# Performance work log

Hardware: AMD Instinct MI355X
Metric: run time of the kernel (lower is better)

The kernel has to match this reference:

```python
import jax, jax.numpy as jnp
import numpy as np

V, E, G, D = 30000, 60000, 1200, 64
NODE_IN, EDGE_IN, EH = 74, 12, 128
N_MP, N_S2S, N_LSTM = 6, 6, 3


def setup_inputs() -> dict:
    key = jax.random.key(0)
    ks = iter(jax.random.split(key, 48))
    def rn(shape, s=0.05):
        return jax.random.normal(next(ks), shape, dtype=jnp.float32) * s
    inp = {
        "node_feats": jax.random.normal(next(ks), (V, NODE_IN), dtype=jnp.float32),
        "edge_feats": jax.random.normal(next(ks), (E, EDGE_IN), dtype=jnp.float32),
        "src": jax.random.randint(next(ks), (E,), 0, V, dtype=jnp.int32),
        "dst": jax.random.randint(next(ks), (E,), 0, V, dtype=jnp.int32),
        "node_graph_ids": jnp.sort(jax.random.randint(next(ks), (V,), 0, G, dtype=jnp.int32)),
        # MPNNGNN: node projection, edge network, NNConv bias, GRU
        "proj_W": rn((NODE_IN, D)), "proj_b": rn((D,)),
        "eW1": rn((EDGE_IN, EH)), "eb1": rn((EH,)),
        "eW2": rn((EH, D * D)), "eb2": rn((D * D,)),
        "conv_b": rn((D,)),
        "gru_Wih": rn((D, 3 * D)), "gru_bih": rn((3 * D,)),
        "gru_Whh": rn((D, 3 * D)), "gru_bhh": rn((3 * D,)),
        # process + predict MLPs
        "pW": rn((2 * D, D)), "pb": rn((D,)),
        "qW1": rn((D, D)), "qb1": rn((D,)),
        "qW2": rn((D, D)), "qb2": rn((D,)),
        "qW3": rn((D, 1)), "qb3": rn((1,)),
    }
    # Set2Set 3-layer LSTM: layer0 input 2D, layers 1-2 input D; gates i,f,g,o
    for l, din in enumerate([2 * D, D, D]):
        inp[f"lstm_Wih{l}"] = rn((din, 4 * D)); inp[f"lstm_bih{l}"] = rn((4 * D,))
        inp[f"lstm_Whh{l}"] = rn((D, 4 * D)); inp[f"lstm_bhh{l}"] = rn((4 * D,))
    return inp


def _forward(floats, src, dst, gids):
    (node_feats, edge_feats, proj_W, proj_b, eW1, eb1, eW2, eb2, conv_b,
     gru_Wih, gru_bih, gru_Whh, gru_bhh,
     lWih0, lbih0, lWhh0, lbhh0,
     lWih1, lbih1, lWhh1, lbhh1,
     lWih2, lbih2, lWhh2, lbhh2,
     pW, pb, qW1, qb1, qW2, qb2, qW3, qb3) = floats

    # ---- MPNNGNN ----
    h = jax.nn.relu(node_feats @ proj_W + proj_b)            # (V, D)
    hidden = h
    # per-edge weight matrices (edge_feats fixed across MP steps -> compute once)
    We = (jax.nn.relu(edge_feats @ eW1 + eb1) @ eW2 + eb2).reshape(E, D, D)
    for _ in range(N_MP):
        m = jnp.einsum('ei,eio->eo', h[src], We)             # (E, D)
        agg = jax.ops.segment_sum(m, dst, num_segments=V) + conv_b
        x = jax.nn.relu(agg)
        # PyTorch GRU cell
        gi = x @ gru_Wih + gru_bih
        gh = hidden @ gru_Whh + gru_bhh
        ir, iz, inn = jnp.split(gi, 3, axis=-1)
        hr, hz, hn = jnp.split(gh, 3, axis=-1)
        r = jax.nn.sigmoid(ir + hr)
        z = jax.nn.sigmoid(iz + hz)
        n = jnp.tanh(inn + r * hn)
        h = (1.0 - z) * n + z * hidden
        hidden = h

    # ---- Set2Set readout ----
    lstm = [(lWih0, lbih0, lWhh0, lbhh0),
            (lWih1, lbih1, lWhh1, lbhh1),
            (lWih2, lbih2, lWhh2, lbhh2)]
    hs = [jnp.zeros((G, D), h.dtype) for _ in range(N_LSTM)]
    cs = [jnp.zeros((G, D), h.dtype) for _ in range(N_LSTM)]
    q_star = jnp.zeros((G, 2 * D), h.dtype)
    for _ in range(N_S2S):
        x = q_star
        nhs, ncs = [], []
        for l, (Wih, bih, Whh, bhh) in enumerate(lstm):
            gates = x @ Wih + bih + hs[l] @ Whh + bhh
            i_g, f_g, g_g, o_g = jnp.split(gates, 4, axis=-1)
            c = jax.nn.sigmoid(f_g) * cs[l] + jax.nn.sigmoid(i_g) * jnp.tanh(g_g)
            hh = jax.nn.sigmoid(o_g) * jnp.tanh(c)
            nhs.append(hh); ncs.append(c)
            x = hh
        hs, cs = nhs, ncs
        q = x                                               # (G, D)
        e = jnp.sum(h * q[gids], axis=-1)                   # (V,)
        emax = jax.ops.segment_max(e, gids, num_segments=G, indices_are_sorted=True)
        ex = jnp.exp(e - emax[gids])
        denom = jax.ops.segment_sum(ex, gids, num_segments=G, indices_are_sorted=True)
        alpha = ex / denom[gids]                            # per-graph softmax
        readout = jax.ops.segment_sum(h * alpha[:, None], gids, num_segments=G, indices_are_sorted=True)
        q_star = jnp.concatenate([q, readout], axis=-1)     # (G, 2D)

    # ---- process + predict MLPs (dropout = identity in eval) ----
    gf = jax.nn.relu(q_star @ pW + pb)
    y = jax.nn.relu(gf @ qW1 + qb1)
    y = jax.nn.relu(y @ qW2 + qb2)
    return y @ qW3 + qb3                                    # (G, 1)


def reference(node_feats, edge_feats, src, dst, node_graph_ids,
              proj_W, proj_b, eW1, eb1, eW2, eb2, conv_b,
              gru_Wih, gru_bih, gru_Whh, gru_bhh,
              lstm_Wih0, lstm_bih0, lstm_Whh0, lstm_bhh0,
              lstm_Wih1, lstm_bih1, lstm_Whh1, lstm_bhh1,
              lstm_Wih2, lstm_bih2, lstm_Whh2, lstm_bhh2,
              pW, pb, qW1, qb1, qW2, qb2, qW3, qb3):
    floats = (node_feats, edge_feats, proj_W, proj_b, eW1, eb1, eW2, eb2, conv_b,
              gru_Wih, gru_bih, gru_Whh, gru_bhh,
              lstm_Wih0, lstm_bih0, lstm_Whh0, lstm_bhh0,
              lstm_Wih1, lstm_bih1, lstm_Whh1, lstm_bhh1,
              lstm_Wih2, lstm_bih2, lstm_Whh2, lstm_bhh2,
              pW, pb, qW1, qb1, qW2, qb2, qW3, qb3)
    return _forward(floats, src, dst, node_graph_ids)
```

## Files before the change

### kernel.cpp

```cpp
#include <hip/hip_runtime.h>
#include <stdint.h>
#include <math.h>

#define V 30000
#define E 60000
#define G 1200
#define D 64
#define NODE_IN 74
#define EDGE_IN 12
#define EH 128
#define N_MP 6
#define N_S2S 6

#define NBLK ((E + 63) / 64)
#define EPAD (NBLK * 64)
#define GRUBLK ((V + 31) / 32)

typedef short bf16x8 __attribute__((ext_vector_type(8)));
typedef float f32x4 __attribute__((ext_vector_type(4)));

__device__ __forceinline__ float sigmoidf_(float x) {
    return 1.0f / (1.0f + __expf(-x));
}
__device__ __forceinline__ float tanhf_(float x) {
    float t = __expf(-2.0f * fabsf(x));
    float r = (1.0f - t) / (1.0f + t);
    return copysignf(r, x);
}
__device__ __forceinline__ uint16_t f2bf(float f) {
    uint32_t u = __float_as_uint(f);
    u += 0x7fffu + ((u >> 16) & 1u);
    return (uint16_t)(u >> 16);
}
__device__ __forceinline__ float bf2f(uint16_t u) {
    return __uint_as_float(((uint32_t)u) << 16);
}

__global__ void k_zero(float* __restrict__ p, int n4) {
    int i = blockIdx.x * blockDim.x + threadIdx.x;
    if (i < n4) ((float4*)p)[i] = make_float4(0.f, 0.f, 0.f, 0.f);
}

__global__ void k_node_proj(const float* __restrict__ nf, const float* __restrict__ W,
                            const float* __restrict__ b, float* __restrict__ h) {
    int wave = threadIdx.x >> 6, lane = threadIdx.x & 63;
    int v = blockIdx.x * 4 + wave;
    __shared__ float xs[4][NODE_IN];
    xs[wave][lane] = nf[(size_t)v * NODE_IN + lane];
    if (lane + 64 < NODE_IN) xs[wave][lane + 64] = nf[(size_t)v * NODE_IN + lane + 64];
    __syncthreads();
    float acc = b[lane];
    #pragma unroll
    for (int i = 0; i < NODE_IN; ++i) acc = fmaf(xs[wave][i], W[i * D + lane], acc);
    h[(size_t)v * D + lane] = fmaxf(acc, 0.0f);
}

__global__ __launch_bounds__(256) void k_edge_hidden(const float* __restrict__ ef,
                              const float* __restrict__ W1,
                              const float* __restrict__ b1, uint16_t* __restrict__ HedgeP) {
    int blk = blockIdx.x;
    int t = threadIdx.x;
    int half = t >> 7, j = t & 127;
    __shared__ float xs[8][EDGE_IN];
    if (t < 8 * EDGE_IN) {
        int el = t / EDGE_IN, c = t % EDGE_IN;
        int e = blk * 8 + el;
        xs[el][c] = (e < E) ? ef[(size_t)e * EDGE_IN + c] : 0.f;
    }
    __syncthreads();
    #pragma unroll
    for (int l = 0; l < 4; ++l) {
        int el = half * 4 + l;
        int e = blk * 8 + el;
        float acc = b1[j];
        #pragma unroll
        for (int i = 0; i < EDGE_IN; ++i) acc = fmaf(xs[el][i], W1[i * EH + j], acc);
        float r = (e < E) ? fmaxf(acc, 0.0f) : 0.0f;
        int bb = e >> 6, ww = (e >> 4) & 3, m = e & 15;
        int kt = j >> 5, quad = (j >> 3) & 3, jj = j & 7;
        size_t off = ((((size_t)(bb * 4 + ww) * 4 + kt) * 4 + quad) * 16 + m) * 8 + jj;
        HedgeP[off] = f2bf(r);
    }
}

__global__ void k_prep_w2(const float* __restrict__ eW2, uint16_t* __restrict__ W2p) {
    int idx = blockIdx.x * 256 + threadIdx.x;
    int j = idx & 7;
    int n0 = (idx >> 3) & 15;
    int quad = (idx >> 7) & 3;
    int nt = (idx >> 9) & 3;
    int kt = (idx >> 11) & 3;
    int i = idx >> 13;
    int k = kt * 32 + quad * 8 + j;
    int col = i * 64 + nt * 16 + n0;
    W2p[idx] = f2bf(eW2[(size_t)k * 4096 + col]);
}

__global__ void k_prep_b2(const float* __restrict__ eb2, uint16_t* __restrict__ B2p) {
    int idx = blockIdx.x * 256 + threadIdx.x;
    if (idx >= 4096) { B2p[idx] = 0; return; }
    int j = idx & 7;
    int n0 = (idx >> 3) & 15;
    int quad = (idx >> 7) & 3;
    int nt = (idx >> 9) & 3;
    int kb = (idx >> 11) & 1;
    B2p[idx] = f2bf(eb2[(size_t)(kb * 32 + quad * 8 + j) * 64 + nt * 16 + n0]);
}

__global__ void k_prep_wc(const float* __restrict__ Wih, const float* __restrict__ Whh,
                          const float* __restrict__ bih, const float* __restrict__ bhh,
                          uint16_t* __restrict__ Wcp, float* __restrict__ bc) {
    int idx = blockIdx.x * 256 + threadIdx.x;
    int j = idx & 7;
    int n0 = (idx >> 3) & 15;
    int quad = (idx >> 7) & 3;
    int kt = (idx >> 9) & 3;
    int ot = idx >> 11;
    int k = kt * 32 + quad * 8 + j;
    int c = ot * 16 + n0;
    float val = 0.f;
    if (c < 128) {
        val = (k < 64) ? Wih[(size_t)k * 192 + c] : Whh[(size_t)(k - 64) * 192 + c];
    } else if (c < 192) {
        if (k < 64) val = Wih[(size_t)k * 192 + c];
    } else {
        if (k >= 64) val = Whh[(size_t)(k - 64) * 192 + (c - 64)];
    }
    Wcp[idx] = f2bf(val);
    if (idx < 256) {
        int d = idx & 63;
        float b;
        if (idx < 64)       b = bih[d] + bhh[d];
        else if (idx < 128) b = bih[64 + d] + bhh[64 + d];
        else if (idx < 192) b = bih[128 + d];
        else                b = bhh[128 + d];
        bc[idx] = b;
    }
}

__global__ __launch_bounds__(256, 3) void k_message_mfma(
    const uint16_t* __restrict__ HedgeP, const uint16_t* __restrict__ W2p,
    const uint16_t* __restrict__ B2p, const float* __restrict__ h,
    const int* __restrict__ src, const int* __restrict__ dst,
    float* __restrict__ agg) {
    const int bx = blockIdx.x;
    const int b = bx >> 1;
    const int ibase = (bx & 1) * 32;
    const int t = threadIdx.x;
    const int w = t >> 6, lane = t & 63;
    const int quad = lane >> 4, n0 = lane & 15;

    __shared__ uint16_t HsU[64][72];
    __shared__ int srcv[64], dstv[64];

    if (t < 64) {
        int e = b * 64 + t;
        int sv = 0, dv = -1;
        if (e < E) { sv = src[e]; dv = dst[e]; }
        srcv[t] = sv; dstv[t] = dv;
    }
    __syncthreads();
    for (int idx = t; idx < 4096; idx += 256) {
        int r = idx >> 6, c = idx & 63;
        HsU[r][c] = f2bf(h[(size_t)srcv[r] * 64 + c]);
    }
    bf16x8 Af[4][4];
    #pragma unroll
    for (int et = 0; et < 4; ++et)
        #pragma unroll
        for (int kt = 0; kt < 4; ++kt)
            Af[et][kt] = *(const bf16x8*)(HedgeP + (((size_t)(b * 4 + et) * 4 + kt) * 512) + lane * 8);
    __syncthreads();

    f32x4 acc[4];
    {
        const uint16_t* b2b = B2p + (size_t)ibase * 128;
        bf16x8 B2f0 = *(const bf16x8*)(b2b + (size_t)(0 * 4 + w) * 512 + lane * 8);
        bf16x8 B2f1 = *(const bf16x8*)(b2b + (size_t)(1 * 4 + w) * 512 + lane * 8);
        #pragma unroll
        for (int et = 0; et < 4; ++et) {
            bf16x8 hA0 = *(const bf16x8*)(&HsU[et * 16 + n0][quad * 8]);
            bf16x8 hA1 = *(const bf16x8*)(&HsU[et * 16 + n0][32 + quad * 8]);
            f32x4 z = {};
            z = __builtin_amdgcn_mfma_f32_16x16x32_bf16(hA0, B2f0, z, 0, 0, 0);
            acc[et] = __builtin_amdgcn_mfma_f32_16x16x32_bf16(hA1, B2f1, z, 0, 0, 0);
        }
    }

    for (int ii = 0; ii < 32; ++ii) {
        const int i = ibase + ii;
        const uint16_t* wb = W2p + (size_t)i * 8192 + lane * 8;
        bf16x8 Bf0 = *(const bf16x8*)(wb + (size_t)(0 * 4 + w) * 512);
        bf16x8 Bf1 = *(const bf16x8*)(wb + (size_t)(1 * 4 + w) * 512);
        bf16x8 Bf2 = *(const bf16x8*)(wb + (size_t)(2 * 4 + w) * 512);
        bf16x8 Bf3 = *(const bf16x8*)(wb + (size_t)(3 * 4 + w) * 512);
        #pragma unroll
        for (int et = 0; et < 4; ++et) {
            f32x4 tmp = {};
            tmp = __builtin_amdgcn_mfma_f32_16x16x32_bf16(Af[et][0], Bf0, tmp, 0, 0, 0);
            tmp = __builtin_amdgcn_mfma_f32_16x16x32_bf16(Af[et][1], Bf1, tmp, 0, 0, 0);
            tmp = __builtin_amdgcn_mfma_f32_16x16x32_bf16(Af[et][2], Bf2, tmp, 0, 0, 0);
            tmp = __builtin_amdgcn_mfma_f32_16x16x32_bf16(Af[et][3], Bf3, tmp, 0, 0, 0);
            int r0 = et * 16 + quad * 4;
            acc[et][0] = fmaf(bf2f(HsU[r0 + 0][i]), tmp[0], acc[et][0]);
            acc[et][1] = fmaf(bf2f(HsU[r0 + 1][i]), tmp[1], acc[et][1]);
            acc[et][2] = fmaf(bf2f(HsU[r0 + 2][i]), tmp[2], acc[et][2]);
            acc[et][3] = fmaf(bf2f(HsU[r0 + 3][i]), tmp[3], acc[et][3]);
        }
    }

    #pragma unroll
    for (int et = 0; et < 4; ++et) {
        #pragma unroll
        for (int reg = 0; reg < 4; ++reg) {
            int d = dstv[et * 16 + quad * 4 + reg];
            if (d >= 0)
                atomicAdd(agg + (size_t)d * 64 + w * 16 + n0, acc[et][reg]);
        }
    }
}

__global__ __launch_bounds__(256) void k_gru_mfma(
    float* __restrict__ agg, const float* __restrict__ convb,
    const uint16_t* __restrict__ Wcp, const float* __restrict__ bc,
    float* __restrict__ hcur) {
    const int blk = blockIdx.x;
    const int v0 = blk * 32;
    const int t = threadIdx.x;
    const int w = t >> 6, lane = t & 63;
    const int quad = lane >> 4, n0 = lane & 15;

    __shared__ uint16_t As[32][136];
    __shared__ uint16_t Gs[32][264];

    for (int idx = t; idx < 2048; idx += 256) {
        int r = idx >> 6, c = idx & 63;
        int v = v0 + r;
        if (v < V) {
            size_t off = (size_t)v * 64 + c;
            float x = fmaxf(agg[off] + convb[c], 0.f);
            agg[off] = 0.f;
            As[r][c] = f2bf(x);
            As[r][64 + c] = f2bf(hcur[off]);
        } else {
            As[r][c] = 0; As[r][64 + c] = 0;
        }
    }
    __syncthreads();

    bf16x8 Af[2][4];
    #pragma unroll
    for (int et = 0; et < 2; ++et)
        #pragma unroll
        for (int kt = 0; kt < 4; ++kt)
            Af[et][kt] = *(const bf16x8*)(&As[et * 16 + n0][kt * 32 + quad * 8]);

    f32x4 acc[2][4] = {};
    #pragma unroll
    for (int ot4 = 0; ot4 < 4; ++ot4) {
        const uint16_t* wb = Wcp + (size_t)((w * 4 + ot4) * 4) * 512 + lane * 8;
        bf16x8 B0 = *(const bf16x8*)(wb + 0 * 512);
        bf16x8 B1 = *(const bf16x8*)(wb + 1 * 512);
        bf16x8 B2 = *(const bf16x8*)(wb + 2 * 512);
        bf16x8 B3 = *(const bf16x8*)(wb + 3 * 512);
        #pragma unroll
        for (int et = 0; et < 2; ++et) {
            f32x4 a = acc[et][ot4];
            a = __builtin_amdgcn_mfma_f32_16x16x32_bf16(Af[et][0], B0, a, 0, 0, 0);
            a = __builtin_amdgcn_mfma_f32_16x16x32_bf16(Af[et][1], B1, a, 0, 0, 0);
            a = __builtin_amdgcn_mfma_f32_16x16x32_bf16(Af[et][2], B2, a, 0, 0, 0);
            a = __builtin_amdgcn_mfma_f32_16x16x32_bf16(Af[et][3], B3, a, 0, 0, 0);
            acc[et][ot4] = a;
        }
    }
    #pragma unroll
    for (int et = 0; et < 2; ++et)
        #pragma unroll
        for (int ot4 = 0; ot4 < 4; ++ot4)
            #pragma unroll
            for (int reg = 0; reg < 4; ++reg)
                Gs[et * 16 + quad * 4 + reg][(w * 4 + ot4) * 16 + n0] = f2bf(acc[et][ot4][reg]);
    __syncthreads();

    for (int idx = t; idx < 2048; idx += 256) {
        int r = idx >> 6, d = idx & 63;
        int v = v0 + r;
        if (v >= V) continue;
        size_t off = (size_t)v * 64 + d;
        float rp   = bf2f(Gs[r][d])        + bc[d];
        float zp   = bf2f(Gs[r][64 + d])   + bc[64 + d];
        float innv = bf2f(Gs[r][128 + d])  + bc[128 + d];
        float hnv  = bf2f(Gs[r][192 + d])  + bc[192 + d];
        float hv = hcur[off];
        float rr = sigmoidf_(rp);
        float zz = sigmoidf_(zp);
        float nn = tanhf_(innv + rr * hnv);
        hcur[off] = (1.f - zz) * nn + zz * hv;
    }
}

__global__ void k_seg(const int* __restrict__ gids, int* __restrict__ start) {
    int v = blockIdx.x * blockDim.x + threadIdx.x;
    if (v > V) return;
    int cur = (v < V) ? gids[v] : G;
    int prev = (v == 0) ? -1 : gids[v - 1];
    for (int g = prev + 1; g <= cur; ++g) start[g] = v;
}

#define LS_GPB 8
__global__ __launch_bounds__(256) void k_lstm(const float* __restrict__ q_star,
    const float* __restrict__ Wih0, const float* __restrict__ bih0,
    const float* __restrict__ Whh0, const float* __restrict__ bhh0,
    const float* __restrict__ Wih1, const float* __restrict__ bih1,
    const float* __restrict__ Whh1, const float* __restrict__ bhh1,
    const float* __restrict__ Wih2, const float* __restrict__ bih2,
    const float* __restrict__ Whh2, const float* __restrict__ bhh2,
    float* __restrict__ hs, float* __restrict__ cs, float* __restrict__ q) {
    int g0 = blockIdx.x * LS_GPB;
    int j = threadIdx.x;
    __shared__ float xs[LS_GPB][128];
    __shared__ float hl[LS_GPB][64];
    __shared__ float gates[LS_GPB][256];
    for (int idx = j; idx < LS_GPB * 128; idx += 256) {
        int n = idx >> 7, d = idx & 127;
        xs[n][d] = q_star[(size_t)(g0 + n) * 128 + d];
    }
    const float* Wihs[3] = {Wih0, Wih1, Wih2};
    const float* bihs[3] = {bih0, bih1, bih2};
    const float* Whhs[3] = {Whh0, Whh1, Whh2};
    const float* bhhs[3] = {bhh0, bhh1, bhh2};
    const int dins[3] = {128, 64, 64};
    for (int l = 0; l < 3; ++l) {
        for (int idx = j; idx < LS_GPB * 64; idx += 256) {
            int n = idx >> 6, d = idx & 63;
            hl[n][d] = hs[(size_t)l * G * 64 + (size_t)(g0 + n) * 64 + d];
        }
        __syncthreads();
        float acc[LS_GPB];
        float bsum = bihs[l][j] + bhhs[l][j];
        #pragma unroll
        for (int n = 0; n < LS_GPB; ++n) acc[n] = bsum;
        const float* Wih = Wihs[l];
        int din = dins[l];
        for (int i = 0; i < din; ++i) {
            float w = Wih[i * 256 + j];
            #pragma unroll
            for (int n = 0; n < LS_GPB; ++n) acc[n] = fmaf(xs[n][i], w, acc[n]);
        }
        const float* Whh = Whhs[l];
        for (int i = 0; i < 64; ++i) {
            float w = Whh[i * 256 + j];
            #pragma unroll
            for (int n = 0; n < LS_GPB; ++n) acc[n] = fmaf(hl[n][i], w, acc[n]);
        }
        #pragma unroll
        for (int n = 0; n < LS_GPB; ++n) gates[n][j] = acc[n];
        __syncthreads();
        for (int idx = j; idx < LS_GPB * 64; idx += 256) {
            int n = idx >> 6, d = idx & 63;
            float ig = gates[n][d], fg = gates[n][64 + d];
            float gt = gates[n][128 + d], og = gates[n][192 + d];
            size_t off = (size_t)l * G * 64 + (size_t)(g0 + n) * 64 + d;
            float c = sigmoidf_(fg) * cs[off] + sigmoidf_(ig) * tanhf_(gt);
            float hnew = sigmoidf_(og) * tanhf_(c);
            cs[off] = c;
            hs[off] = hnew;
            xs[n][d] = hnew;
            if (l == 2) q[(size_t)(g0 + n) * 64 + d] = hnew;
        }
        __syncthreads();
    }
}

__global__ void k_attention(const float* __restrict__ h, const float* __restrict__ q,
                            const int* __restrict__ segs, float* __restrict__ q_star) {
    int g = blockIdx.x;
    int lane = threadIdx.x;
    int vs = segs[g], ve = segs[g + 1];
    float qv = q[(size_t)g * 64 + lane];
    float m = -INFINITY;
    for (int v = vs; v < ve; ++v) {
        float p = h[(size_t)v * 64 + lane] * qv;
        #pragma unroll
        for (int off = 32; off > 0; off >>= 1) p += __shfl_xor(p, off, 64);
        m = fmaxf(m, p);
    }
    float s = 0.f, acc = 0.f;
    for (int v = vs; v < ve; ++v) {
        float hv = h[(size_t)v * 64 + lane];
        float p = hv * qv;
        #pragma unroll
        for (int off = 32; off > 0; off >>= 1) p += __shfl_xor(p, off, 64);
        float ex = __expf(p - m);
        s += ex;
        acc = fmaf(hv, ex, acc);
    }
    float r = (ve > vs) ? acc / s : 0.f;
    q_star[(size_t)g * 128 + lane] = qv;
    q_star[(size_t)g * 128 + 64 + lane] = r;
}

__global__ void k_final(const float* __restrict__ q_star,
                        const float* __restrict__ pW, const float* __restrict__ pb,
                        const float* __restrict__ qW1, const float* __restrict__ qb1,
                        const float* __restrict__ qW2, const float* __restrict__ qb2,
                        const float* __restrict__ qW3, const float* __restrict__ qb3,
                        float* __restrict__ out) {
    int g = blockIdx.x;
    int lane = threadIdx.x;
    __shared__ float buf[128];
    buf[lane] = q_star[(size_t)g * 128 + lane];
    buf[64 + lane] = q_star[(size_t)g * 128 + 64 + lane];
    __syncthreads();
    float y = pb[lane];
    #pragma unroll 8
    for (int i = 0; i < 128; ++i) y = fmaf(buf[i], pW[i * 64 + lane], y);
    y = fmaxf(y, 0.f);
    __syncthreads(); buf[lane] = y; __syncthreads();
    float y1 = qb1[lane];
    #pragma unroll 8
    for (int i = 0; i < 64; ++i) y1 = fmaf(buf[i], qW1[i * 64 + lane], y1);
    y1 = fmaxf(y1, 0.f);
    __syncthreads(); buf[lane] = y1; __syncthreads();
    float y2 = qb2[lane];
    #pragma unroll 8
    for (int i = 0; i < 64; ++i) y2 = fmaf(buf[i], qW2[i * 64 + lane], y2);
    y2 = fmaxf(y2, 0.f);
    float p = y2 * qW3[lane];
    #pragma unroll
    for (int off = 32; off > 0; off >>= 1) p += __shfl_xor(p, off, 64);
    if (lane == 0) out[g] = p + qb3[0];
}

extern "C" void kernel_launch(void* const* d_in, const int* in_sizes, int n_in,
                              void* d_out, int out_size, void* d_ws, size_t ws_size,
                              hipStream_t stream) {
    const float* node_feats = (const float*)d_in[0];
    const float* edge_feats = (const float*)d_in[1];
    const int*   src        = (const int*)d_in[2];
    const int*   dst        = (const int*)d_in[3];
    const int*   gids       = (const int*)d_in[4];
    const float* proj_W     = (const float*)d_in[5];
    const float* proj_b     = (const float*)d_in[6];
    const float* eW1        = (const float*)d_in[7];
    const float* eb1        = (const float*)d_in[8];
    const float* eW2        = (const float*)d_in[9];
    const float* eb2        = (const float*)d_in[10];
    const float* conv_b     = (const float*)d_in[11];
    const float* gru_Wih    = (const float*)d_in[12];
    const float* gru_bih    = (const float*)d_in[13];
    const float* gru_Whh    = (const float*)d_in[14];
    const float* gru_bhh    = (const float*)d_in[15];
    const float* pW         = (const float*)d_in[16];
    const float* pb         = (const float*)d_in[17];
    const float* qW1        = (const float*)d_in[18];
    const float* qb1        = (const float*)d_in[19];
    const float* qW2        = (const float*)d_in[20];
    const float* qb2        = (const float*)d_in[21];
    const float* qW3        = (const float*)d_in[22];
    const float* qb3        = (const float*)d_in[23];
    const float* lWih0 = (const float*)d_in[24]; const float* lbih0 = (const float*)d_in[25];
    const float* lWhh0 = (const float*)d_in[26]; const float* lbhh0 = (const float*)d_in[27];
    const float* lWih1 = (const float*)d_in[28]; const float* lbih1 = (const float*)d_in[29];
    const float* lWhh1 = (const float*)d_in[30]; const float* lbhh1 = (const float*)d_in[31];
    const float* lWih2 = (const float*)d_in[32]; const float* lbih2 = (const float*)d_in[33];
    const float* lWhh2 = (const float*)d_in[34]; const float* lbhh2 = (const float*)d_in[35];

    char* ws = (char*)d_ws;
    uint16_t* HedgeP = (uint16_t*)(ws + 0);
    uint16_t* W2p    = (uint16_t*)(ws + 15368192);
    uint16_t* B2p    = (uint16_t*)(ws + 16416768);
    float*    hcur   = (float*)(ws + 16433152);
    float*    agg    = (float*)(ws + 24113152);
    float*    q_star = (float*)(ws + 31793152);
    float*    hsbuf  = (float*)(ws + 32407552);
    float*    csbuf  = (float*)(ws + 33329152);
    float*    qbuf   = (float*)(ws + 34250752);
    int*      segs   = (int*)(ws + 34557952);
    uint16_t* Wcp    = (uint16_t*)hsbuf;
    float*    bc     = (float*)(ws + 32407552 + 65536);

    k_node_proj<<<V / 4, 256, 0, stream>>>(node_feats, proj_W, proj_b, hcur);
    k_edge_hidden<<<EPAD / 8, 256, 0, stream>>>(edge_feats, eW1, eb1, HedgeP);
    k_prep_w2<<<2048, 256, 0, stream>>>(eW2, W2p);
    k_prep_b2<<<32, 256, 0, stream>>>(eb2, B2p);
    k_prep_wc<<<128, 256, 0, stream>>>(gru_Wih, gru_Whh, gru_bih, gru_bhh, Wcp, bc);
    k_seg<<<(V + 1 + 255) / 256, 256, 0, stream>>>(gids, segs);
    k_zero<<<(480000 + 255) / 256, 256, 0, stream>>>(agg, 480000);

    for (int t = 0; t < N_MP; ++t) {
        k_message_mfma<<<NBLK * 2, 256, 0, stream>>>(HedgeP, W2p, B2p, hcur, src, dst, agg);
        k_gru_mfma<<<GRUBLK, 256, 0, stream>>>(agg, conv_b, Wcp, bc, hcur);
    }

    k_zero<<<(153600 + 255) / 256, 256, 0, stream>>>(q_star, 153600);

    for (int s = 0; s < N_S2S; ++s) {
        k_lstm<<<G / LS_GPB, 256, 0, stream>>>(q_star,
            lWih0, lbih0, lWhh0, lbhh0,
            lWih1, lbih1, lWhh1, lbhh1,
            lWih2, lbih2, lWhh2, lbhh2,
            hsbuf, csbuf, qbuf);
        k_attention<<<G, 64, 0, stream>>>(hcur, qbuf, segs, q_star);
    }

    k_final<<<G, 64, 0, stream>>>(q_star, pW, pb, qW1, qb1, qW2, qb2, qW3, qb3,
                                  (float*)d_out);
}
```

Baseline: 1.020 ms.

## Fuse Set2Set LSTM, attention and final MLP into one persistent kernel

Replaces the 6 rounds of separate LSTM and attention launches, the q_star zeroing and the final MLP kernel with a single kernel that keeps LSTM state and q_star in shared memory across all Set2Set steps. Attention now uses an online softmax, so each node row is read in one pass instead of two. This removes about 13 kernel launches and the global round-trips of the LSTM state. In exchange only 150 blocks run the attention (two graphs per wave, done one after another), which lowers parallelism in that phase.

Measured after the change: 954.0 us. 6.4% less time.

```diff
diff --git a/kernel.cpp b/kernel.cpp
--- a/kernel.cpp
+++ b/kernel.cpp
@@ -308,128 +308,127 @@
 }
 
 #define LS_GPB 8
-__global__ __launch_bounds__(256) void k_lstm(const float* __restrict__ q_star,
+__global__ __launch_bounds__(256) void k_s2s_final(
+    const float* __restrict__ h, const int* __restrict__ segs,
     const float* __restrict__ Wih0, const float* __restrict__ bih0,
     const float* __restrict__ Whh0, const float* __restrict__ bhh0,
     const float* __restrict__ Wih1, const float* __restrict__ bih1,
     const float* __restrict__ Whh1, const float* __restrict__ bhh1,
     const float* __restrict__ Wih2, const float* __restrict__ bih2,
     const float* __restrict__ Whh2, const float* __restrict__ bhh2,
-    float* __restrict__ hs, float* __restrict__ cs, float* __restrict__ q) {
-    int g0 = blockIdx.x * LS_GPB;
-    int j = threadIdx.x;
+    const float* __restrict__ pW, const float* __restrict__ pb,
+    const float* __restrict__ qW1, const float* __restrict__ qb1,
+    const float* __restrict__ qW2, const float* __restrict__ qb2,
+    const float* __restrict__ qW3, const float* __restrict__ qb3,
+    float* __restrict__ out) {
+    const int g0 = blockIdx.x * LS_GPB;
+    const int j = threadIdx.x;
+    const int w = j >> 6, lane = j & 63;
+
     __shared__ float xs[LS_GPB][128];
-    __shared__ float hl[LS_GPB][64];
+    __shared__ float hsL[3][LS_GPB][64];
+    __shared__ float csL[3][LS_GPB][64];
     __shared__ float gates[LS_GPB][256];
-    for (int idx = j; idx < LS_GPB * 128; idx += 256) {
-        int n = idx >> 7, d = idx & 127;
-        xs[n][d] = q_star[(size_t)(g0 + n) * 128 + d];
-    }
+    __shared__ float qst[LS_GPB][128];
+
+    for (int idx = j; idx < LS_GPB * 64 * 3; idx += 256) {
+        ((float*)hsL)[idx] = 0.f;
+        ((float*)csL)[idx] = 0.f;
+    }
+    for (int idx = j; idx < LS_GPB * 128; idx += 256) ((float*)qst)[idx] = 0.f;
+    __syncthreads();
+
     const float* Wihs[3] = {Wih0, Wih1, Wih2};
     const float* bihs[3] = {bih0, bih1, bih2};
     const float* Whhs[3] = {Whh0, Whh1, Whh2};
     const float* bhhs[3] = {bhh0, bhh1, bhh2};
     const int dins[3] = {128, 64, 64};
-    for (int l = 0; l < 3; ++l) {
-        for (int idx = j; idx < LS_GPB * 64; idx += 256) {
-            int n = idx >> 6, d = idx & 63;
-            hl[n][d] = hs[(size_t)l * G * 64 + (size_t)(g0 + n) * 64 + d];
+
+    for (int s = 0; s < N_S2S; ++s) {
+        for (int idx = j; idx < LS_GPB * 128; idx += 256) {
+            int n = idx >> 7, d = idx & 127;
+            xs[n][d] = qst[n][d];
         }
         __syncthreads();
-        float acc[LS_GPB];
-        float bsum = bihs[l][j] + bhhs[l][j];
-        #pragma unroll
-        for (int n = 0; n < LS_GPB; ++n) acc[n] = bsum;
-        const float* Wih = Wihs[l];
-        int din = dins[l];
-        for (int i = 0; i < din; ++i) {
-            float w = Wih[i * 256 + j];
+        for (int l = 0; l < 3; ++l) {
+            float acc[LS_GPB];
+            float bsum = bihs[l][j] + bhhs[l][j];
             #pragma unroll
-            for (int n = 0; n < LS_GPB; ++n) acc[n] = fmaf(xs[n][i], w, acc[n]);
-        }
-        const float* Whh = Whhs[l];
-        for (int i = 0; i < 64; ++i) {
-            float w = Whh[i * 256 + j];
+            for (int n = 0; n < LS_GPB; ++n) acc[n] = bsum;
+            const float* Wih = Wihs[l];
+            int din = dins[l];
+            for (int i = 0; i < din; ++i) {
+                float wv = Wih[i * 256 + j];
+                #pragma unroll
+                for (int n = 0; n < LS_GPB; ++n) acc[n] = fmaf(xs[n][i], wv, acc[n]);
+            }
+            const float* Whh = Whhs[l];
+            for (int i = 0; i < 64; ++i) {
+                float wv = Whh[i * 256 + j];
+                #pragma unroll
+                for (int n = 0; n < LS_GPB; ++n) acc[n] = fmaf(hsL[l][n][i], wv, acc[n]);
+            }
             #pragma unroll
-            for (int n = 0; n < LS_GPB; ++n) acc[n] = fmaf(hl[n][i], w, acc[n]);
-        }
-        #pragma unroll
-        for (int n = 0; n < LS_GPB; ++n) gates[n][j] = acc[n];
+            for (int n = 0; n < LS_GPB; ++n) gates[n][j] = acc[n];
+            __syncthreads();
+            for (int idx = j; idx < LS_GPB * 64; idx += 256) {
+                int n = idx >> 6, d = idx & 63;
+                float ig = gates[n][d], fg = gates[n][64 + d];
+                float gt = gates[n][128 + d], og = gates[n][192 + d];
+                float c = sigmoidf_(fg) * csL[l][n][d] + sigmoidf_(ig) * tanhf_(gt);
+                float hnew = sigmoidf_(og) * tanhf_(c);
+                csL[l][n][d] = c;
+                hsL[l][n][d] = hnew;
+                xs[n][d] = hnew;
+            }
+            __syncthreads();
+        }
+        #pragma unroll
+        for (int gi = 0; gi < 2; ++gi) {
+            int gg = w + gi * 4;
+            int g = g0 + gg;
+            float qd = xs[gg][lane];
+            int vs = segs[g], ve = segs[g + 1];
+            float m = -INFINITY, sden = 0.f, accd = 0.f;
+            for (int v = vs; v < ve; ++v) {
+                float hv = h[(size_t)v * 64 + lane];
+                float p = hv * qd;
+                #pragma unroll
+                for (int off = 32; off > 0; off >>= 1) p += __shfl_xor(p, off, 64);
+                float nm = fmaxf(m, p);
+                float e1 = __expf(m - nm);
+                float e2 = __expf(p - nm);
+                sden = sden * e1 + e2;
+                accd = accd * e1 + hv * e2;
+                m = nm;
+            }
+            float r = (ve > vs) ? accd / sden : 0.f;
+            qst[gg][lane] = qd;
+            qst[gg][64 + lane] = r;
+        }
         __syncthreads();
-        for (int idx = j; idx < LS_GPB * 64; idx += 256) {
-            int n = idx >> 6, d = idx & 63;
-            float ig = gates[n][d], fg = gates[n][64 + d];
-            float gt = gates[n][128 + d], og = gates[n][192 + d];
-            size_t off = (size_t)l * G * 64 + (size_t)(g0 + n) * 64 + d;
-            float c = sigmoidf_(fg) * cs[off] + sigmoidf_(ig) * tanhf_(gt);
-            float hnew = sigmoidf_(og) * tanhf_(c);
-            cs[off] = c;
-            hs[off] = hnew;
-            xs[n][d] = hnew;
-            if (l == 2) q[(size_t)(g0 + n) * 64 + d] = hnew;
-        }
-        __syncthreads();
-    }
-}
-
-__global__ void k_attention(const float* __restrict__ h, const float* __restrict__ q,
-                            const int* __restrict__ segs, float* __restrict__ q_star) {
-    int g = blockIdx.x;
-    int lane = threadIdx.x;
-    int vs = segs[g], ve = segs[g + 1];
-    float qv = q[(size_t)g * 64 + lane];
-    float m = -INFINITY;
-    for (int v = vs; v < ve; ++v) {
-        float p = h[(size_t)v * 64 + lane] * qv;
+    }
+
+    #pragma unroll
+    for (int gi = 0; gi < 2; ++gi) {
+        int gg = w + gi * 4;
+        int g = g0 + gg;
+        float y = pb[lane];
+        for (int i = 0; i < 128; ++i) y = fmaf(qst[gg][i], pW[i * 64 + lane], y);
+        y = fmaxf(y, 0.f);
+        gates[gg][lane] = y;
+        float y1 = qb1[lane];
+        for (int i = 0; i < 64; ++i) y1 = fmaf(gates[gg][i], qW1[i * 64 + lane], y1);
+        y1 = fmaxf(y1, 0.f);
+        gates[gg][64 + lane] = y1;
+        float y2 = qb2[lane];
+        for (int i = 0; i < 64; ++i) y2 = fmaf(gates[gg][64 + i], qW2[i * 64 + lane], y2);
+        y2 = fmaxf(y2, 0.f);
+        float p = y2 * qW3[lane];
         #pragma unroll
         for (int off = 32; off > 0; off >>= 1) p += __shfl_xor(p, off, 64);
-        m = fmaxf(m, p);
-    }
-    float s = 0.f, acc = 0.f;
-    for (int v = vs; v < ve; ++v) {
-        float hv = h[(size_t)v * 64 + lane];
-        float p = hv * qv;
-        #pragma unroll
-        for (int off = 32; off > 0; off >>= 1) p += __shfl_xor(p, off, 64);
-        float ex = __expf(p - m);
-        s += ex;
-        acc = fmaf(hv, ex, acc);
-    }
-    float r = (ve > vs) ? acc / s : 0.f;
-    q_star[(size_t)g * 128 + lane] = qv;
-    q_star[(size_t)g * 128 + 64 + lane] = r;
-}
-
-__global__ void k_final(const float* __restrict__ q_star,
-                        const float* __restrict__ pW, const float* __restrict__ pb,
-                        const float* __restrict__ qW1, const float* __restrict__ qb1,
-                        const float* __restrict__ qW2, const float* __restrict__ qb2,
-                        const float* __restrict__ qW3, const float* __restrict__ qb3,
-                        float* __restrict__ out) {
-    int g = blockIdx.x;
-    int lane = threadIdx.x;
-    __shared__ float buf[128];
-    buf[lane] = q_star[(size_t)g * 128 + lane];
-    buf[64 + lane] = q_star[(size_t)g * 128 + 64 + lane];
-    __syncthreads();
-    float y = pb[lane];
-    #pragma unroll 8
-    for (int i = 0; i < 128; ++i) y = fmaf(buf[i], pW[i * 64 + lane], y);
-    y = fmaxf(y, 0.f);
-    __syncthreads(); buf[lane] = y; __syncthreads();
-    float y1 = qb1[lane];
-    #pragma unroll 8
-    for (int i = 0; i < 64; ++i) y1 = fmaf(buf[i], qW1[i * 64 + lane], y1);
-    y1 = fmaxf(y1, 0.f);
-    __syncthreads(); buf[lane] = y1; __syncthreads();
-    float y2 = qb2[lane];
-    #pragma unroll 8
-    for (int i = 0; i < 64; ++i) y2 = fmaf(buf[i], qW2[i * 64 + lane], y2);
-    y2 = fmaxf(y2, 0.f);
-    float p = y2 * qW3[lane];
-    #pragma unroll
-    for (int off = 32; off > 0; off >>= 1) p += __shfl_xor(p, off, 64);
-    if (lane == 0) out[g] = p + qb3[0];
+        if (lane == 0) out[g] = p + qb3[0];
+    }
 }
 
 extern "C" void kernel_launch(void* const* d_in, const int* in_sizes, int n_in,
@@ -472,12 +471,8 @@
     uint16_t* B2p    = (uint16_t*)(ws + 16416768);
     float*    hcur   = (float*)(ws + 16433152);
     float*    agg    = (float*)(ws + 24113152);
-    float*    q_star = (float*)(ws + 31793152);
-    float*    hsbuf  = (float*)(ws + 32407552);
-    float*    csbuf  = (float*)(ws + 33329152);
-    float*    qbuf   = (float*)(ws + 34250752);
     int*      segs   = (int*)(ws + 34557952);
-    uint16_t* Wcp    = (uint16_t*)hsbuf;
+    uint16_t* Wcp    = (uint16_t*)(ws + 32407552);
     float*    bc     = (float*)(ws + 32407552 + 65536);
 
     k_node_proj<<<V / 4, 256, 0, stream>>>(node_feats, proj_W, proj_b, hcur);
@@ -493,17 +488,10 @@
         k_gru_mfma<<<GRUBLK, 256, 0, stream>>>(agg, conv_b, Wcp, bc, hcur);
     }
 
-    k_zero<<<(153600 + 255) / 256, 256, 0, stream>>>(q_star, 153600);
-
-    for (int s = 0; s < N_S2S; ++s) {
-        k_lstm<<<G / LS_GPB, 256, 0, stream>>>(q_star,
-            lWih0, lbih0, lWhh0, lbhh0,
-            lWih1, lbih1, lWhh1, lbhh1,
-            lWih2, lbih2, lWhh2, lbhh2,
-            hsbuf, csbuf, qbuf);
-        k_attention<<<G, 64, 0, stream>>>(hcur, qbuf, segs, q_star);
-    }
-
-    k_final<<<G, 64, 0, stream>>>(q_star, pW, pb, qW1, qb1, qW2, qb2, qW3, qb3,
-                                  (float*)d_out);
-}
+    k_s2s_final<<<G / LS_GPB, 256, 0, stream>>>(hcur, segs,
+        lWih0, lbih0, lWhh0, lbhh0,
+        lWih1, lbih1, lWhh1, lbhh1,
+        lWih2, lbih2, lWhh2, lbhh2,
+        pW, pb, qW1, qb1, qW2, qb2, qW3, qb3,
+        (float*)d_out);
+}
```
